# Performance work log

Hardware: AMD Instinct MI355X
Metric: run time of the kernel (lower is better)

Reference implementation:

```python
import jax, jax.numpy as jnp
import numpy as np

B, S, D = 2, 2048, 1024
H = 16
HD = D // H  # 64


def setup_inputs() -> dict:
    key = jax.random.key(0)
    k = jax.random.split(key, 6)
    s = 0.02
    return {
        "x": jax.random.normal(k[0], (B, S, D), dtype=jnp.float32),
        "wq": jax.random.normal(k[1], (D, D), dtype=jnp.float32) * s,
        "wk": jax.random.normal(k[2], (D, D), dtype=jnp.float32) * s,
        "wv": jax.random.normal(k[3], (D, D), dtype=jnp.float32) * s,
        "wo": jax.random.normal(k[4], (D, D), dtype=jnp.float32) * s,
        "bo": jnp.zeros((D,), dtype=jnp.float32),
    }


def reference(x, wq, wk, wv, wo, bo):
    b, n, d = x.shape
    # nn.Linear: y = x @ W.T (qkv_bias=False)
    def proj(w):
        y = jnp.einsum('bnd,od->bno', x, w)
        return y.reshape(b, n, H, HD).transpose(0, 2, 1, 3)  # (b, H, n, hd)
    q, k, v = proj(wq), proj(wk), proj(wv)
    scores = jnp.einsum('bhqd,bhkd->bhqk', q, k) / jnp.sqrt(jnp.float32(HD))
    # NOTE: source code slices the causal mask but never applies it; softmax is unmasked.
    attn = jax.nn.softmax(scores, axis=-1)
    # dropout p=0.0 -> identity
    ctx = jnp.einsum('bhqk,bhkd->bhqd', attn, v)
    ctx = ctx.transpose(0, 2, 1, 3).reshape(b, n, d)
    return jnp.einsum('bnd,od->bno', ctx, wo) + bo
```

## Files before the change

kernel.cpp:

```cpp
#include <hip/hip_runtime.h>
#include <hip/hip_bf16.h>
#include <stdint.h>

typedef __attribute__((ext_vector_type(8))) short short8;
typedef __attribute__((ext_vector_type(4))) float float4v;
typedef __attribute__((ext_vector_type(4))) unsigned short ushort4v;

#define Bq 2
#define Sq 2048
#define Dq 1024
#define Hq 16
#define HDq 64

__device__ __forceinline__ unsigned short f2bf(float f) {
  union { float f; uint32_t u; } v; v.f = f;
  uint32_t r = (v.u + 0x7FFFu + ((v.u >> 16) & 1u)) >> 16;
  return (unsigned short)r;
}

__device__ __forceinline__ uint32_t pk2bf(float a, float b) {
  union { __hip_bfloat162 h; uint32_t u; } cv;
  cv.h = __float22bfloat162_rn(make_float2(a, b));
  return cv.u;
}

__device__ __forceinline__ void gl_lds16(const unsigned short* g, unsigned short* l) {
  __builtin_amdgcn_global_load_lds(
      (const __attribute__((address_space(1))) void*)g,
      (__attribute__((address_space(3))) void*)l, 16, 0, 0);
}

__global__ __launch_bounds__(256) void cvt_all_kernel(
    const float* __restrict__ x,
    const float* __restrict__ w0, const float* __restrict__ w1,
    const float* __restrict__ w2, const float* __restrict__ w3,
    unsigned short* __restrict__ xb, unsigned short* __restrict__ wb) {
  const int bid = blockIdx.x;
  const float* src;
  unsigned short* dst;
  int idx;
  if (bid < 4096) {
    idx = bid * 256 + threadIdx.x;
    src = x; dst = xb;
  } else {
    int j = (bid - 4096) * 256 + threadIdx.x;
    int z = j >> 18;
    src = (z == 0) ? w0 : (z == 1) ? w1 : (z == 2) ? w2 : w3;
    src -= (size_t)z * 1048576;
    idx = j; dst = wb;
    src = (z == 0) ? w0 - 0 : src;
    src = (z == 0) ? w0 : (z == 1) ? w1 : (z == 2) ? w2 : w3;
    idx = j & 262143;
    dst = wb + (size_t)(j >> 18) * 1048576 / 1;
    dst = wb + (size_t)(j >> 18) * 1048576;
    float4v f = ((const float4v*)src)[idx];
    ushort4v o;
#pragma unroll
    for (int q = 0; q < 4; q++) o[q] = f2bf(f[q]);
    ((ushort4v*)dst)[idx] = o;
    return;
  }
  float4v f = ((const float4v*)src)[idx];
  ushort4v o;
#pragma unroll
  for (int q = 0; q < 4; q++) o[q] = f2bf(f[q]);
  ((ushort4v*)dst)[idx] = o;
}

template <bool OUTPROJ, int MT>
__global__ __launch_bounds__(256) void gemm_bt_kernel(
    const unsigned short* __restrict__ A,
    const unsigned short* __restrict__ W0,
    const unsigned short* __restrict__ W1,
    const unsigned short* __restrict__ W2,
    unsigned short* __restrict__ q_dst,
    unsigned short* __restrict__ k_dst,
    unsigned short* __restrict__ v_dst,
    float* __restrict__ f_dst,
    const float* __restrict__ bias) {
  constexpr int K = 1024;
  constexpr int NMB = MT / 32;
  const int z = blockIdx.z;
  const unsigned short* W = (z == 0) ? W0 : (z == 1) ? W1 : W2;
  unsigned short* qkv = (z == 0) ? q_dst : (z == 1) ? k_dst : v_dst;

  __shared__ unsigned short Asm[MT * 32];
  __shared__ unsigned short Bsm[128 * 32];

  const int t = threadIdx.x;
  const int wave = t >> 6, lane = t & 63;
  const int quad = lane >> 4, l16 = lane & 15;
  const int wy = wave >> 1, wx = wave & 1;
  const int row0 = blockIdx.x * MT;
  const int col0 = blockIdx.y * 128;

  float4v zero = {0.f, 0.f, 0.f, 0.f};
  float4v acc[NMB][4];
#pragma unroll
  for (int i = 0; i < NMB; i++)
#pragma unroll
    for (int j = 0; j < 4; j++) acc[i][j] = zero;

  const int sr = t >> 2;
  const int sc = (t & 3) << 3;
  const unsigned short* ga = A + (size_t)(row0 + sr) * K + sc;
  const unsigned short* gb = W + (size_t)(col0 + sr) * K + sc;

  for (int k0 = 0; k0 < K; k0 += 32) {
    gl_lds16(ga + k0, &Asm[t * 8]);
    if constexpr (MT == 128) gl_lds16(ga + (size_t)64 * K + k0, &Asm[2048 + t * 8]);
    gl_lds16(gb + k0, &Bsm[t * 8]);
    gl_lds16(gb + (size_t)64 * K + k0, &Bsm[2048 + t * 8]);
    __syncthreads();
    short8 af[NMB], bf[4];
#pragma unroll
    for (int mb = 0; mb < NMB; mb++)
      af[mb] = *(const short8*)(&Asm[(wy * (MT / 2) + mb * 16 + l16) * 32 + quad * 8]);
#pragma unroll
    for (int nb = 0; nb < 4; nb++)
      bf[nb] = *(const short8*)(&Bsm[(wx * 64 + nb * 16 + l16) * 32 + quad * 8]);
#pragma unroll
    for (int mb = 0; mb < NMB; mb++)
#pragma unroll
      for (int nb = 0; nb < 4; nb++)
        acc[mb][nb] = __builtin_amdgcn_mfma_f32_16x16x32_bf16(af[mb], bf[nb], acc[mb][nb], 0, 0, 0);
    __syncthreads();
  }

#pragma unroll
  for (int mb = 0; mb < NMB; mb++) {
#pragma unroll
    for (int nb = 0; nb < 4; nb++) {
#pragma unroll
      for (int r = 0; r < 4; r++) {
        int row = row0 + wy * (MT / 2) + mb * 16 + quad * 4 + r;
        int o = col0 + wx * 64 + nb * 16 + l16;
        float val = acc[mb][nb][r];
        if (OUTPROJ) {
          f_dst[(size_t)row * 1024 + o] = val + bias[o];
        } else {
          int b = row >> 11, s = row & 2047;
          int h = o >> 6, hd = o & 63;
          qkv[(size_t)((b * Hq + h) * Sq + s) * HDq + hd] = f2bf(val);
        }
      }
    }
  }
}

__global__ __launch_bounds__(256) void attn_kernel(
    const unsigned short* __restrict__ Q,
    const unsigned short* __restrict__ Kg,
    const unsigned short* __restrict__ Vg,
    unsigned short* __restrict__ ctx) {
  constexpr int KSTR = 68;
  constexpr int VSTR = 136;
  const int bh = blockIdx.y;
  const int q0 = blockIdx.x * 128;
  const int t = threadIdx.x;
  const int wave = t >> 6, lane = t & 63;
  const int quad = lane >> 4, l16 = lane & 15;

  __shared__ unsigned short Ksm[128 * KSTR];
  __shared__ unsigned short Vsm[64 * VSTR];

  const unsigned short* Qb = Q + (size_t)bh * Sq * HDq;
  const unsigned short* Kb = Kg + (size_t)bh * Sq * HDq;
  const unsigned short* Vb = Vg + (size_t)bh * Sq * HDq;

  short8 qf[2][2];
#pragma unroll
  for (int rb = 0; rb < 2; rb++)
#pragma unroll
    for (int ks = 0; ks < 2; ks++)
      qf[rb][ks] = *(const short8*)(Qb + (size_t)(q0 + wave * 32 + rb * 16 + l16) * HDq + ks * 32 + quad * 8);

  float4v zero = {0.f, 0.f, 0.f, 0.f};
  float4v of[2][4];
  float lsum[2] = {0.f, 0.f};
#pragma unroll
  for (int rb = 0; rb < 2; rb++)
#pragma unroll
    for (int hb = 0; hb < 4; hb++) of[rb][hb] = zero;

  const int kr0 = t >> 3, kc = (t & 7) << 3;
  const int vr2 = (t & 63) * 2;
  const int vc8 = (t >> 6) << 3;
  const int sig = (vr2 & ~31) + (((vr2 >> 2) & 3) << 3) + (((vr2 >> 4) & 1) << 2) + (vr2 & 3);

  short8 kpr[4], vpr0[2], vpr1[2];
#pragma unroll
  for (int i = 0; i < 4; i++)
    kpr[i] = *(const short8*)(Kb + (size_t)(kr0 + i * 32) * HDq + kc);
#pragma unroll
  for (int i = 0; i < 2; i++) {
    vpr0[i] = *(const short8*)(Vb + (size_t)vr2 * HDq + vc8 + i * 32);
    vpr1[i] = *(const short8*)(Vb + (size_t)(vr2 + 1) * HDq + vc8 + i * 32);
  }

  for (int kt = 0; kt < Sq; kt += 128) {
#pragma unroll
    for (int i = 0; i < 4; i++)
      *(short8*)(&Ksm[(kr0 + i * 32) * KSTR + kc]) = kpr[i];
#pragma unroll
    for (int i = 0; i < 2; i++)
#pragma unroll
      for (int j = 0; j < 8; j++) {
        uint32_t pk = (uint32_t)(unsigned short)vpr0[i][j] |
                      ((uint32_t)(unsigned short)vpr1[i][j] << 16);
        *(uint32_t*)(&Vsm[(vc8 + i * 32 + j) * VSTR + sig]) = pk;
      }
    __syncthreads();

    if (kt + 128 < Sq) {
      const unsigned short* Kn = Kb + (size_t)(kt + 128) * HDq;
      const unsigned short* Vn = Vb + (size_t)(kt + 128) * HDq;
#pragma unroll
      for (int i = 0; i < 4; i++)
        kpr[i] = *(const short8*)(Kn + (size_t)(kr0 + i * 32) * HDq + kc);
#pragma unroll
      for (int i = 0; i < 2; i++) {
        vpr0[i] = *(const short8*)(Vn + (size_t)vr2 * HDq + vc8 + i * 32);
        vpr1[i] = *(const short8*)(Vn + (size_t)(vr2 + 1) * HDq + vc8 + i * 32);
      }
    }

#pragma unroll
    for (int p = 0; p < 4; p++) {
      float4v sf[2][2];
#pragma unroll
      for (int rb = 0; rb < 2; rb++)
#pragma unroll
        for (int s = 0; s < 2; s++) sf[rb][s] = zero;
#pragma unroll
      for (int s = 0; s < 2; s++)
#pragma unroll
        for (int ks = 0; ks < 2; ks++) {
          short8 kf = *(const short8*)(&Ksm[(p * 32 + s * 16 + l16) * KSTR + ks * 32 + quad * 8]);
#pragma unroll
          for (int rb = 0; rb < 2; rb++)
            sf[rb][s] = __builtin_amdgcn_mfma_f32_16x16x32_bf16(kf, qf[rb][ks], sf[rb][s], 0, 0, 0);
        }
      short8 pf[2];
#pragma unroll
      for (int rb = 0; rb < 2; rb++) {
        union { uint32_t u[4]; short8 v; } pw;
#pragma unroll
        for (int s = 0; s < 2; s++)
#pragma unroll
          for (int rp = 0; rp < 2; rp++) {
            float pa = __expf(sf[rb][s][rp * 2] * 0.125f);
            float pb = __expf(sf[rb][s][rp * 2 + 1] * 0.125f);
            lsum[rb] += pa + pb;
            pw.u[s * 2 + rp] = pk2bf(pa, pb);
          }
        pf[rb] = pw.v;
      }
#pragma unroll
      for (int hb = 0; hb < 4; hb++) {
        short8 vf = *(const short8*)(&Vsm[(hb * 16 + l16) * VSTR + p * 32 + quad * 8]);
#pragma unroll
        for (int rb = 0; rb < 2; rb++)
          of[rb][hb] = __builtin_amdgcn_mfma_f32_16x16x32_bf16(pf[rb], vf, of[rb][hb], 0, 0, 0);
      }
    }
    __syncthreads();
  }

  float dinv[2][4];
#pragma unroll
  for (int rb = 0; rb < 2; rb++) {
    float l = lsum[rb];
    l += __shfl_xor(l, 16, 64);
    l += __shfl_xor(l, 32, 64);
#pragma unroll
    for (int r = 0; r < 4; r++)
      dinv[rb][r] = 1.0f / __shfl(l, quad * 4 + r, 64);
  }

  const int b = bh >> 4, h = bh & 15;
#pragma unroll
  for (int rb = 0; rb < 2; rb++)
#pragma unroll
    for (int hb = 0; hb < 4; hb++)
#pragma unroll
      for (int r = 0; r < 4; r++) {
        int srow = q0 + wave * 32 + rb * 16 + quad * 4 + r;
        int d = h * 64 + hb * 16 + l16;
        ctx[(size_t)(b * Sq + srow) * Dq + d] = f2bf(of[rb][hb][r] * dinv[rb][r]);
      }
}

extern "C" void kernel_launch(void* const* d_in, const int* in_sizes, int n_in,
                              void* d_out, int out_size, void* d_ws, size_t ws_size,
                              hipStream_t stream) {
  (void)in_sizes; (void)n_in; (void)out_size; (void)ws_size;
  const float* x  = (const float*)d_in[0];
  const float* wq = (const float*)d_in[1];
  const float* wk = (const float*)d_in[2];
  const float* wv = (const float*)d_in[3];
  const float* wo = (const float*)d_in[4];
  const float* bo = (const float*)d_in[5];
  float* out = (float*)d_out;

  char* ws = (char*)d_ws;
  const size_t MB = 1u << 20;
  unsigned short* xb  = (unsigned short*)(ws + 0 * MB);
  unsigned short* wqb = (unsigned short*)(ws + 8 * MB);
  unsigned short* wkb = (unsigned short*)(ws + 10 * MB);
  unsigned short* wvb = (unsigned short*)(ws + 12 * MB);
  unsigned short* wob = (unsigned short*)(ws + 14 * MB);
  unsigned short* qb  = (unsigned short*)(ws + 16 * MB);
  unsigned short* kb  = (unsigned short*)(ws + 24 * MB);
  unsigned short* vb  = (unsigned short*)(ws + 32 * MB);
  unsigned short* cxb = (unsigned short*)(ws + 40 * MB);

  cvt_all_kernel<<<8192, 256, 0, stream>>>(x, wq, wk, wv, wo, xb, wqb);

  gemm_bt_kernel<false, 128><<<dim3(32, 8, 3), 256, 0, stream>>>(
      xb, wqb, wkb, wvb, qb, kb, vb, nullptr, nullptr);
  attn_kernel<<<dim3(16, 32), 256, 0, stream>>>(qb, kb, vb, cxb);
  gemm_bt_kernel<true, 64><<<dim3(64, 8, 1), 256, 0, stream>>>(
      cxb, wob, wob, wob, nullptr, nullptr, nullptr, out, bo);
}
```

Measured before the change: 190.5 us.

## Widen GEMM K-tile with swizzled LDS, fold softmax scale into Q, MFMA rowsum

The projection GEMM now stages 64-wide K slices with an XOR-swizzled LDS layout, which halves the number of barrier-separated iterations and is meant to avoid LDS bank conflicts. The Q projection epilogue pre-multiplies by scale*log2(e), so attention can use the raw exp2 instruction instead of __expf with a multiply. The softmax denominator is now accumulated with an extra MFMA against a vector of bf16 ones, replacing scalar adds and cross-lane shuffles. The conversion kernel is also tidied up. Costs: doubled LDS per block, and a row sum taken from bf16-rounded probabilities, which shifts numerics slightly; there is still no running-max subtraction.

```diff
diff --git a/kernel.cpp b/kernel.cpp
--- a/kernel.cpp
+++ b/kernel.cpp
@@ -11,6 +11,8 @@
 #define Dq 1024
 #define Hq 16
 #define HDq 64
+
+#define QSCALE 0.18033688011112042f
 
 __device__ __forceinline__ unsigned short f2bf(float f) {
   union { float f; uint32_t u; } v; v.f = f;
@@ -40,25 +42,14 @@
   unsigned short* dst;
   int idx;
   if (bid < 4096) {
+    src = x; dst = xb;
     idx = bid * 256 + threadIdx.x;
-    src = x; dst = xb;
   } else {
     int j = (bid - 4096) * 256 + threadIdx.x;
     int z = j >> 18;
     src = (z == 0) ? w0 : (z == 1) ? w1 : (z == 2) ? w2 : w3;
-    src -= (size_t)z * 1048576;
-    idx = j; dst = wb;
-    src = (z == 0) ? w0 - 0 : src;
-    src = (z == 0) ? w0 : (z == 1) ? w1 : (z == 2) ? w2 : w3;
+    dst = wb + (size_t)z * 1048576;
     idx = j & 262143;
-    dst = wb + (size_t)(j >> 18) * 1048576 / 1;
-    dst = wb + (size_t)(j >> 18) * 1048576;
-    float4v f = ((const float4v*)src)[idx];
-    ushort4v o;
-#pragma unroll
-    for (int q = 0; q < 4; q++) o[q] = f2bf(f[q]);
-    ((ushort4v*)dst)[idx] = o;
-    return;
   }
   float4v f = ((const float4v*)src)[idx];
   ushort4v o;
@@ -80,12 +71,13 @@
     const float* __restrict__ bias) {
   constexpr int K = 1024;
   constexpr int NMB = MT / 32;
+  constexpr int APASS = MT / 32;
   const int z = blockIdx.z;
   const unsigned short* W = (z == 0) ? W0 : (z == 1) ? W1 : W2;
   unsigned short* qkv = (z == 0) ? q_dst : (z == 1) ? k_dst : v_dst;
 
-  __shared__ unsigned short Asm[MT * 32];
-  __shared__ unsigned short Bsm[128 * 32];
+  __shared__ unsigned short Asm[MT * 64];
+  __shared__ unsigned short Bsm[128 * 64];
 
   const int t = threadIdx.x;
   const int wave = t >> 6, lane = t & 63;
@@ -101,32 +93,52 @@
 #pragma unroll
     for (int j = 0; j < 4; j++) acc[i][j] = zero;
 
-  const int sr = t >> 2;
-  const int sc = (t & 3) << 3;
-  const unsigned short* ga = A + (size_t)(row0 + sr) * K + sc;
-  const unsigned short* gb = W + (size_t)(col0 + sr) * K + sc;
-
-  for (int k0 = 0; k0 < K; k0 += 32) {
-    gl_lds16(ga + k0, &Asm[t * 8]);
-    if constexpr (MT == 128) gl_lds16(ga + (size_t)64 * K + k0, &Asm[2048 + t * 8]);
-    gl_lds16(gb + k0, &Bsm[t * 8]);
-    gl_lds16(gb + (size_t)64 * K + k0, &Bsm[2048 + t * 8]);
+  const int srow = t >> 3;
+  const int sgl = ((t & 7) ^ (srow & 7)) << 3;
+  const unsigned short* gA[APASS];
+  const unsigned short* gB[4];
+#pragma unroll
+  for (int i = 0; i < APASS; i++)
+    gA[i] = A + (size_t)(row0 + i * 32 + srow) * K + sgl;
+#pragma unroll
+  for (int i = 0; i < 4; i++)
+    gB[i] = W + (size_t)(col0 + i * 32 + srow) * K + sgl;
+
+  const int swl = (l16 & 7);
+
+  for (int k0 = 0; k0 < K; k0 += 64) {
+#pragma unroll
+    for (int i = 0; i < APASS; i++) gl_lds16(gA[i] + k0, &Asm[i * 2048 + t * 8]);
+#pragma unroll
+    for (int i = 0; i < 4; i++) gl_lds16(gB[i] + k0, &Bsm[i * 2048 + t * 8]);
     __syncthreads();
-    short8 af[NMB], bf[4];
-#pragma unroll
-    for (int mb = 0; mb < NMB; mb++)
-      af[mb] = *(const short8*)(&Asm[(wy * (MT / 2) + mb * 16 + l16) * 32 + quad * 8]);
-#pragma unroll
-    for (int nb = 0; nb < 4; nb++)
-      bf[nb] = *(const short8*)(&Bsm[(wx * 64 + nb * 16 + l16) * 32 + quad * 8]);
-#pragma unroll
-    for (int mb = 0; mb < NMB; mb++)
-#pragma unroll
-      for (int nb = 0; nb < 4; nb++)
-        acc[mb][nb] = __builtin_amdgcn_mfma_f32_16x16x32_bf16(af[mb], bf[nb], acc[mb][nb], 0, 0, 0);
+    short8 af[NMB][2], bf[4][2];
+#pragma unroll
+    for (int ks = 0; ks < 2; ks++) {
+#pragma unroll
+      for (int mb = 0; mb < NMB; mb++) {
+        int row = wy * (MT / 2) + mb * 16 + l16;
+        int pg = (ks * 4 + quad) ^ swl;
+        af[mb][ks] = *(const short8*)(&Asm[row * 64 + pg * 8]);
+      }
+#pragma unroll
+      for (int nb = 0; nb < 4; nb++) {
+        int row = wx * 64 + nb * 16 + l16;
+        int pg = (ks * 4 + quad) ^ swl;
+        bf[nb][ks] = *(const short8*)(&Bsm[row * 64 + pg * 8]);
+      }
+    }
+#pragma unroll
+    for (int ks = 0; ks < 2; ks++)
+#pragma unroll
+      for (int mb = 0; mb < NMB; mb++)
+#pragma unroll
+        for (int nb = 0; nb < 4; nb++)
+          acc[mb][nb] = __builtin_amdgcn_mfma_f32_16x16x32_bf16(af[mb][ks], bf[nb][ks], acc[mb][nb], 0, 0, 0);
     __syncthreads();
   }
 
+  const float qsc = (!OUTPROJ && z == 0) ? QSCALE : 1.0f;
 #pragma unroll
   for (int mb = 0; mb < NMB; mb++) {
 #pragma unroll
@@ -141,7 +153,7 @@
         } else {
           int b = row >> 11, s = row & 2047;
           int h = o >> 6, hd = o & 63;
-          qkv[(size_t)((b * Hq + h) * Sq + s) * HDq + hd] = f2bf(val);
+          qkv[(size_t)((b * Hq + h) * Sq + s) * HDq + hd] = f2bf(val * qsc);
         }
       }
     }
@@ -175,9 +187,13 @@
     for (int ks = 0; ks < 2; ks++)
       qf[rb][ks] = *(const short8*)(Qb + (size_t)(q0 + wave * 32 + rb * 16 + l16) * HDq + ks * 32 + quad * 8);
 
+  short8 ones;
+#pragma unroll
+  for (int j = 0; j < 8; j++) ones[j] = (short)0x3F80;
+
   float4v zero = {0.f, 0.f, 0.f, 0.f};
   float4v of[2][4];
-  float lsum[2] = {0.f, 0.f};
+  float4v dsum[2] = {zero, zero};
 #pragma unroll
   for (int rb = 0; rb < 2; rb++)
 #pragma unroll
@@ -249,14 +265,16 @@
         for (int s = 0; s < 2; s++)
 #pragma unroll
           for (int rp = 0; rp < 2; rp++) {
-            float pa = __expf(sf[rb][s][rp * 2] * 0.125f);
-            float pb = __expf(sf[rb][s][rp * 2 + 1] * 0.125f);
-            lsum[rb] += pa + pb;
+            float pa = __builtin_amdgcn_exp2f(sf[rb][s][rp * 2]);
+            float pb = __builtin_amdgcn_exp2f(sf[rb][s][rp * 2 + 1]);
             pw.u[s * 2 + rp] = pk2bf(pa, pb);
           }
         pf[rb] = pw.v;
       }
 #pragma unroll
+      for (int rb = 0; rb < 2; rb++)
+        dsum[rb] = __builtin_amdgcn_mfma_f32_16x16x32_bf16(pf[rb], ones, dsum[rb], 0, 0, 0);
+#pragma unroll
       for (int hb = 0; hb < 4; hb++) {
         short8 vf = *(const short8*)(&Vsm[(hb * 16 + l16) * VSTR + p * 32 + quad * 8]);
 #pragma unroll
@@ -267,28 +285,21 @@
     __syncthreads();
   }
 
-  float dinv[2][4];
+  const int b = bh >> 4, h = bh & 15;
 #pragma unroll
   for (int rb = 0; rb < 2; rb++) {
-    float l = lsum[rb];
-    l += __shfl_xor(l, 16, 64);
-    l += __shfl_xor(l, 32, 64);
-#pragma unroll
-    for (int r = 0; r < 4; r++)
-      dinv[rb][r] = 1.0f / __shfl(l, quad * 4 + r, 64);
-  }
-
-  const int b = bh >> 4, h = bh & 15;
-#pragma unroll
-  for (int rb = 0; rb < 2; rb++)
+    float4v dinv;
+#pragma unroll
+    for (int r = 0; r < 4; r++) dinv[r] = 1.0f / dsum[rb][r];
 #pragma unroll
     for (int hb = 0; hb < 4; hb++)
 #pragma unroll
       for (int r = 0; r < 4; r++) {
         int srow = q0 + wave * 32 + rb * 16 + quad * 4 + r;
         int d = h * 64 + hb * 16 + l16;
-        ctx[(size_t)(b * Sq + srow) * Dq + d] = f2bf(of[rb][hb][r] * dinv[rb][r]);
-      }
+        ctx[(size_t)(b * Sq + srow) * Dq + d] = f2bf(of[rb][hb][r] * dinv[r]);
+      }
+  }
 }
 
 extern "C" void kernel_launch(void* const* d_in, const int* in_sizes, int n_in,
```

After: 187.0 us. Within noise of the previous version (-1.8%).
